# Optimization experiments

Measured on AMD Instinct MI355X. Metric: run time of the kernel, lower is better.

Reference implementation:

```python
import jax, jax.numpy as jnp
import numpy as np

B = 65536
V = 7          # vertices
OPD = 48       # op_embedding_dim
ND = 48        # node_embedding_dim
HID = 96       # hid_dim
GD = 128       # gcn out dim
NOPS = 32      # op embedding table size
NONE_OP = 3
MLP_DIMS = [200, 200, 200]


def _flow(y, adj, op_emb, W, attW, attb, bias):
    # DenseGraphFlow: support = y @ W; out = sigmoid(op_emb @ attW + attb) * (adj @ support) + support + bias
    support = jnp.einsum('bvi,io->bvo', y, W)
    gate = jax.nn.sigmoid(jnp.einsum('bve,eo->bvo', op_emb, attW) + attb)
    return gate * jnp.einsum('bvw,bwo->bvo', adj, support) + support + bias


def _forward(x_adj_1, zcp, op_emb_table, input_op_emb, output_op_emb,
             input_node_emb, other_node_emb, xh_W, xh_b,
             gcn0_W, gcn0_attW, gcn0_attb, gcn0_bias,
             gcn_W, gcn_attW, gcn_attb, gcn_bias,
             mlp0_W, mlp0_b, mlp1_W, mlp1_b, mlp2_W, mlp2_b, mlp3_W, mlp3_b,
             x_ops_1):
    b = x_ops_1.shape[0]
    adjs = jnp.transpose(x_adj_1, (0, 2, 1))              # archs use arch.T
    op_inds = x_ops_1[:, 1:-1]                            # [B, V-2]
    mid_op = op_emb_table[op_inds]                        # [B, V-2, OPD]
    op_embs = jnp.concatenate([
        jnp.broadcast_to(input_op_emb[None], (b, 1, OPD)),
        mid_op,
        jnp.broadcast_to(output_op_emb[None], (b, 1, OPD)),
    ], axis=1)                                            # [B, V, OPD]
    node_embs = jnp.concatenate([
        jnp.broadcast_to(input_node_emb[None], (b, 1, ND)),
        jnp.broadcast_to(other_node_emb[None], (b, V - 1, ND)),
    ], axis=1)                                            # [B, V, ND]
    x = jnp.einsum('bvn,nh->bvh', node_embs, xh_W) + xh_b  # [B, V, HID]

    # GCN stack: layer 0 (HID->GD), then 4 layers (GD->GD); relu except last
    y = _flow(x, adjs, op_embs, gcn0_W, gcn0_attW, gcn0_attb, gcn0_bias)
    y = jax.nn.relu(y)
    n_rest = gcn_W.shape[0]
    for i in range(n_rest):
        y = _flow(y, adjs, op_embs, gcn_W[i], gcn_attW[i], gcn_attb[i], gcn_bias[i])
        if i != n_rest - 1:
            y = jax.nn.relu(y)

    # final process: drop input node, mask none-ops, mean over nodes
    y = y[:, 1:, :]                                       # [B, V-1, GD]
    mask = (op_inds != NONE_OP).astype(jnp.float32)[:, :, None]
    y = jnp.concatenate([y[:, :-1, :] * mask, y[:, -1:, :]], axis=1)
    y = jnp.mean(y, axis=1)                               # [B, GD]

    # MLP head (dropout inactive / eval)
    y = jax.nn.relu(y @ mlp0_W + mlp0_b)
    y = jax.nn.relu(y @ mlp1_W + mlp1_b)
    y = jax.nn.relu(y @ mlp2_W + mlp2_b)
    y = y @ mlp3_W + mlp3_b                               # [B, 1]
    return y


def setup_inputs() -> dict:
    key = jax.random.key(0)
    ks = iter(jax.random.split(key, 40))
    u = lambda shape, s: jax.random.uniform(next(ks), shape, jnp.float32, -s, s)
    inp = {}
    inp['x_ops_1'] = jax.random.randint(next(ks), (B, V), 0, NOPS, dtype=jnp.int64)
    inp['x_adj_1'] = jax.random.uniform(next(ks), (B, V, V), jnp.float32)
    inp['zcp'] = jax.random.normal(next(ks), (B, 13), jnp.float32)
    inp['op_emb_table'] = jax.random.normal(next(ks), (NOPS, OPD), jnp.float32)
    inp['input_op_emb'] = jnp.zeros((1, OPD), jnp.float32)
    inp['output_op_emb'] = jax.random.normal(next(ks), (1, OPD), jnp.float32)
    inp['input_node_emb'] = jax.random.normal(next(ks), (1, ND), jnp.float32)
    inp['other_node_emb'] = jnp.zeros((1, ND), jnp.float32)
    inp['xh_W'] = u((ND, HID), 1.0 / np.sqrt(ND))
    inp['xh_b'] = u((HID,), 1.0 / np.sqrt(ND))
    s = 1.0 / np.sqrt(GD)
    inp['gcn0_W'] = u((HID, GD), s)
    inp['gcn0_attW'] = u((OPD, GD), 1.0 / np.sqrt(OPD))
    inp['gcn0_attb'] = u((GD,), 1.0 / np.sqrt(OPD))
    inp['gcn0_bias'] = u((GD,), s)
    inp['gcn_W'] = u((4, GD, GD), s)
    inp['gcn_attW'] = u((4, OPD, GD), 1.0 / np.sqrt(OPD))
    inp['gcn_attb'] = u((4, GD), 1.0 / np.sqrt(OPD))
    inp['gcn_bias'] = u((4, GD), s)
    d = GD
    for i, h in enumerate(MLP_DIMS):
        inp[f'mlp{i}_W'] = u((d, h), 1.0 / np.sqrt(d))
        inp[f'mlp{i}_b'] = u((h,), 1.0 / np.sqrt(d))
        d = h
    inp['mlp3_W'] = u((d, 1), 1.0 / np.sqrt(d))
    inp['mlp3_b'] = u((1,), 1.0 / np.sqrt(d))
    return inp


def reference(x_ops_1, x_adj_1, zcp, op_emb_table, input_op_emb, output_op_emb,
              input_node_emb, other_node_emb, xh_W, xh_b,
              gcn0_W, gcn0_attW, gcn0_attb, gcn0_bias,
              gcn_W, gcn_attW, gcn_attb, gcn_bias,
              mlp0_W, mlp0_b, mlp1_W, mlp1_b, mlp2_W, mlp2_b, mlp3_W, mlp3_b):
    return _forward(x_adj_1, zcp, op_emb_table, input_op_emb, output_op_emb,
                    input_node_emb, other_node_emb, xh_W, xh_b,
                    gcn0_W, gcn0_attW, gcn0_attb, gcn0_bias,
                    gcn_W, gcn_attW, gcn_attb, gcn_bias,
                    mlp0_W, mlp0_b, mlp1_W, mlp1_b, mlp2_W, mlp2_b, mlp3_W, mlp3_b,
                    x_ops_1)
```

## Files before the change

kernel.cpp:

```cpp
#include <hip/hip_runtime.h>
#include <math.h>

#define V 7
#define OPD 48
#define HID 96
#define GD 128
#define NGATE 34
#define NONE_OP 3
#define NB 16

typedef unsigned short u16;
typedef unsigned int u32;
typedef _Float16 f16;
typedef __attribute__((ext_vector_type(4))) _Float16 f16x4;
typedef __attribute__((ext_vector_type(8))) _Float16 f16x8;
typedef __attribute__((ext_vector_type(4))) float f32x4;

#define RSCALE 2048.0f
#define RINV   (1.0f/2048.0f)

#define WS_GATES   0u
#define WS_SUP0T   87040u
#define WS_GWH     91136u
#define WS_GWL     222208u
#define WS_W0H     353280u
#define WS_W0L     406528u
#define WS_W1H     459776u
#define WS_W1L     552960u
#define WS_W2H     646144u
#define WS_W2L     739328u

#define S_YH   0u
#define S_YL   32768u
#define S_SUPT 0u
#define S_ADJ  65536u
#define S_GI   69120u
#define S_TOTAL 69632u
#define S_ZH   0u
#define S_ZL   4096u
#define S_A1H  8192u
#define S_A1L  16384u
#define S_A2H  24576u

__device__ __forceinline__ u32 sw256(u32 row, u32 kb) { return row * 256u + (kb ^ ((row & 7u) << 4)); }
__device__ __forceinline__ u32 sw512(u32 row, u32 kb) { return row * 512u + (kb ^ ((row & 7u) << 4)); }
__device__ __forceinline__ u32 ssw(u32 col, u32 rb) { return col * 512u + (rb ^ (((col ^ (col >> 3)) & 7u) << 4)); }

#define MFMA(a, b, c) __builtin_amdgcn_mfma_f32_16x16x32_f16(a, b, c, 0, 0, 0)

__global__ __launch_bounds__(256) void precompute_kernel(
    const float* __restrict__ op_tbl, const float* __restrict__ in_op,
    const float* __restrict__ out_op, const float* __restrict__ in_node,
    const float* __restrict__ other_node, const float* __restrict__ xh_W,
    const float* __restrict__ xh_b, const float* __restrict__ g0W,
    const float* __restrict__ g0attW, const float* __restrict__ g0attb,
    const float* __restrict__ gattW, const float* __restrict__ gattb,
    const float* __restrict__ gW, const float* __restrict__ m0W,
    const float* __restrict__ m1W, const float* __restrict__ m2W,
    char* __restrict__ ws)
{
  const int blk = blockIdx.x, tid = threadIdx.x;
  float* gates = (float*)(ws + WS_GATES);
  float* sup0T = (float*)(ws + WS_SUP0T);
  if (blk < 85) {
    const int row = blk * 2 + (tid >> 7);
    const int c = tid & 127;
    const int l = row / NGATE, e = row % NGATE;
    const float* emb = (e < 32) ? (op_tbl + e * OPD) : (e == 32 ? in_op : out_op);
    const float* aW = (l == 0) ? g0attW : (gattW + (size_t)(l - 1) * OPD * GD);
    const float* ab = (l == 0) ? g0attb : (gattb + (l - 1) * GD);
    float acc = ab[c];
    for (int j = 0; j < OPD; j++) acc += emb[j] * aW[j * GD + c];
    gates[(size_t)row * GD + c] = 1.0f / (1.0f + expf(-acc));
  } else if (blk == 85) {
    __shared__ float x[V * HID];
    for (int i = tid; i < V * HID; i += 256) {
      const int v = i / HID, h = i % HID;
      const float* emb = (v == 0) ? in_node : other_node;
      float acc = xh_b[h];
      for (int j = 0; j < 48; j++) acc += emb[j] * xh_W[j * HID + h];
      x[i] = acc;
    }
    __syncthreads();
    for (int i = tid; i < V * GD; i += 256) {
      const int v = i / GD, c = i % GD;
      float acc = 0.f;
      for (int h = 0; h < HID; h++) acc += x[v * HID + h] * g0W[h * GD + c];
      sup0T[c * 8 + v] = acc;
    }
    for (int i = tid; i < GD; i += 256) sup0T[i * 8 + 7] = 0.f;
  } else {
    for (int idx = (blk - 86) * 256 + tid; idx < 185344; idx += 128 * 256) {
      float w; f16 *ph, *pl;
      if (idx < 65536) {
        const int l = idx >> 14, rem = idx & 16383;
        const int n = rem >> 7, k = rem & 127;
        w = gW[(size_t)l * 16384 + k * 128 + n];
        ph = (f16*)(ws + WS_GWH) + idx; pl = (f16*)(ws + WS_GWL) + idx;
      } else if (idx < 92160) {
        const int j = idx - 65536, n = j >> 7, k = j & 127;
        w = (n < 200) ? m0W[(size_t)k * 200 + n] : 0.f;
        ph = (f16*)(ws + WS_W0H) + j; pl = (f16*)(ws + WS_W0L) + j;
      } else if (idx < 138752) {
        const int j = idx - 92160, n = j / 224, k = j % 224;
        w = (n < 200 && k < 200) ? m1W[(size_t)k * 200 + n] : 0.f;
        ph = (f16*)(ws + WS_W1H) + j; pl = (f16*)(ws + WS_W1L) + j;
      } else {
        const int j = idx - 138752, n = j / 224, k = j % 224;
        w = (n < 200 && k < 200) ? m2W[(size_t)k * 200 + n] : 0.f;
        ph = (f16*)(ws + WS_W2H) + j; pl = (f16*)(ws + WS_W2L) + j;
      }
      const f16 h = (f16)w;
      *ph = h;
      *pl = (f16)((w - (float)h) * RSCALE);
    }
  }
}

__global__ __launch_bounds__(512, 4) void gin_main_kernel(
    const int* __restrict__ x_ops, const float* __restrict__ x_adj,
    const char* __restrict__ ws,
    const float* __restrict__ g0_bias, const float* __restrict__ gcn_bias,
    const float* __restrict__ m0b, const float* __restrict__ m1b,
    const float* __restrict__ m2b, const float* __restrict__ m3W,
    const float* __restrict__ m3b, float* __restrict__ out)
{
  extern __shared__ char smem[];
  const int tid = threadIdx.x;
  const int bbase = blockIdx.x * NB;
  const float* gates_ws = (const float*)(ws + WS_GATES);
  const float* sup0T = (const float*)(ws + WS_SUP0T);
  const f16* GWH = (const f16*)(ws + WS_GWH);
  const f16* GWL = (const f16*)(ws + WS_GWL);
  const f16* W0H = (const f16*)(ws + WS_W0H);
  const f16* W0L = (const f16*)(ws + WS_W0L);
  const f16* W1H = (const f16*)(ws + WS_W1H);
  const f16* W1L = (const f16*)(ws + WS_W1L);
  const f16* W2H = (const f16*)(ws + WS_W2H);
  const f16* W2L = (const f16*)(ws + WS_W2L);

  for (int i = tid; i < NB * 56; i += 512) {
    const int s = i / 56, r = i % 56, v = r >> 3, w = r & 7;
    ((float*)(smem + S_ADJ))[i] = (w < 7) ? x_adj[(size_t)(bbase + s) * 49 + w * 7 + v] : 0.f;
  }
  if (tid < 128) {
    const int s = tid >> 3, v = tid & 7;
    const int g = (v == 0) ? 32 : (v == 6) ? 33 : (v == 7) ? 0
                : x_ops[(size_t)(bbase + s) * 7 + v];
    ((int*)(smem + S_GI))[tid] = g;
  }
  __syncthreads();

  const int lane = tid & 63, wave = tid >> 6;
  const int lrow = lane & 15, lq = lane >> 4;
  const int ms = tid >> 5;
  const int colbase = (tid & 31) * 4;

  for (int l = 0; l < 5; l++) {
    if (l > 0) {
      const f16* wh = GWH + (l - 1) * 16384;
      const f16* wl = GWL + (l - 1) * 16384;
      f32x4 acc0[8], acc1[8];
#pragma unroll
      for (int t = 0; t < 8; t++) {
        acc0[t] = (f32x4){0.f, 0.f, 0.f, 0.f};
        acc1[t] = (f32x4){0.f, 0.f, 0.f, 0.f};
      }
#pragma unroll
      for (int ks = 0; ks < 4; ks++) {
        const int eo = (wave * 16 + lrow) * 128 + ks * 32 + lq * 8;
        const f16x8 bh = *(const f16x8*)(wh + eo);
        const f16x8 bl = *(const f16x8*)(wl + eo);
#pragma unroll
        for (int t = 0; t < 8; t++) {
          const u32 off = sw256((u32)(t * 16 + lrow), (u32)(ks * 64 + lq * 16));
          const f16x8 ah = *(const f16x8*)(smem + S_YH + off);
          const f16x8 al = *(const f16x8*)(smem + S_YL + off);
          acc0[t] = MFMA(ah, bh, acc0[t]);
          acc1[t] = MFMA(ah, bl, acc1[t]);
          acc1[t] = MFMA(al, bh, acc1[t]);
        }
      }
      __syncthreads();
      {
        const u32 col = (u32)(wave * 16 + lrow);
#pragma unroll
        for (int t = 0; t < 8; t++) {
          f32x4 vv;
#pragma unroll
          for (int r = 0; r < 4; r++) vv[r] = acc0[t][r] + acc1[t][r] * RINV;
          *(f32x4*)(smem + S_SUPT + ssw(col, (u32)(t * 64 + lq * 16))) = vv;
        }
      }
      __syncthreads();
    }

    f32x4 sa[4], sb[4];
    if (l == 0) {
#pragma unroll
      for (int c = 0; c < 4; c++) {
        const float* p = sup0T + (size_t)(colbase + c) * 8;
        sa[c] = *(const f32x4*)p;
        sb[c] = *(const f32x4*)(p + 4);
      }
    } else {
#pragma unroll
      for (int c = 0; c < 4; c++) {
        const u32 col = (u32)(colbase + c);
        sa[c] = *(const f32x4*)(smem + S_SUPT + ssw(col, (u32)(ms * 32)));
        sb[c] = *(const f32x4*)(smem + S_SUPT + ssw(col, (u32)(ms * 32 + 16)));
      }
      __syncthreads();
    }

    {
      const float* bias_l = (l == 0) ? g0_bias : gcn_bias + (l - 1) * GD;
      const f32x4 bb = *(const f32x4*)(bias_l + colbase);
      const int* giv = (const int*)(smem + S_GI) + ms * 8;
      float zacc[4];
#pragma unroll
      for (int c = 0; c < 4; c++) zacc[c] = 0.f;
#pragma unroll
      for (int v = 0; v < 7; v++) {
        const f32x4 a0 = *(const f32x4*)(smem + S_ADJ + (ms * 56 + v * 8) * 4);
        const f32x4 a1 = *(const f32x4*)(smem + S_ADJ + (ms * 56 + v * 8) * 4 + 16);
        const int gidx = giv[v];
        const f32x4 gg = *(const f32x4*)(gates_ws + ((size_t)l * NGATE + gidx) * GD + colbase);
        float y[4];
#pragma unroll
        for (int c = 0; c < 4; c++) {
          const float t = a0[0] * sa[c][0] + a0[1] * sa[c][1] + a0[2] * sa[c][2] + a0[3] * sa[c][3]
                        + a1[0] * sb[c][0] + a1[1] * sb[c][1] + a1[2] * sb[c][2];
          const float sv = (v < 4) ? sa[c][v] : sb[c][v - 4];
          y[c] = gg[c] * t + sv + bb[c];
        }
        if (l < 4) {
          union { f16x4 v4; f16 e[4]; } ph, pl;
#pragma unroll
          for (int c = 0; c < 4; c++) {
            const float r = fmaxf(y[c], 0.f);
            const f16 h = (f16)r;
            ph.e[c] = h;
            pl.e[c] = (f16)((r - (float)h) * RSCALE);
          }
          const u32 yo = sw256((u32)(ms * 8 + v), (u32)(colbase * 2));
          *(f16x4*)(smem + S_YH + yo) = ph.v4;
          *(f16x4*)(smem + S_YL + yo) = pl.v4;
        } else {
          if ((v == 6) || (v >= 1 && gidx != NONE_OP))
#pragma unroll
            for (int c = 0; c < 4; c++) zacc[c] += y[c];
        }
      }
      if (l == 4) {
        union { f16x4 v4; f16 e[4]; } ph, pl;
#pragma unroll
        for (int c = 0; c < 4; c++) {
          const float z = zacc[c] * (1.f / 6.f);
          const f16 h = (f16)z;
          ph.e[c] = h;
          pl.e[c] = (f16)((z - (float)h) * RSCALE);
        }
        const u32 zo = sw256((u32)ms, (u32)(colbase * 2));
        *(f16x4*)(smem + S_ZH + zo) = ph.v4;
        *(f16x4*)(smem + S_ZL + zo) = pl.v4;
        for (int i = tid; i < 6144; i += 512)
          ((u32*)(smem + S_A1H))[i] = 0u;
      }
    }
    __syncthreads();
  }

  {
    f32x4 macc0[2], macc1[2];
#pragma unroll
    for (int i = 0; i < 2; i++) { macc0[i] = (f32x4){0.f,0.f,0.f,0.f}; macc1[i] = (f32x4){0.f,0.f,0.f,0.f}; }
#pragma unroll
    for (int ks = 0; ks < 4; ks++) {
      const u32 off = sw256((u32)lrow, (u32)(ks * 64 + lq * 16));
      const f16x8 zh = *(const f16x8*)(smem + S_ZH + off);
      const f16x8 zl = *(const f16x8*)(smem + S_ZL + off);
#pragma unroll
      for (int i = 0; i < 2; i++) {
        const int nt = wave + i * 8;
        if (nt < 13) {
          const int eo = (nt * 16 + lrow) * 128 + ks * 32 + lq * 8;
          const f16x8 wh8 = *(const f16x8*)(W0H + eo);
          const f16x8 wl8 = *(const f16x8*)(W0L + eo);
          macc0[i] = MFMA(zh, wh8, macc0[i]);
          macc1[i] = MFMA(zh, wl8, macc1[i]);
          macc1[i] = MFMA(zl, wh8, macc1[i]);
        }
      }
    }
#pragma unroll
    for (int i = 0; i < 2; i++) {
      const int nt = wave + i * 8;
      if (nt < 13) {
        const int col = nt * 16 + lrow;
        const float b = (col < 200) ? m0b[col] : 0.f;
#pragma unroll
        for (int r = 0; r < 4; r++) {
          const float a = fmaxf(macc0[i][r] + macc1[i][r] * RINV + b, 0.f);
          const f16 h = (f16)a;
          const u32 off = sw512((u32)(lq * 4 + r), (u32)(2 * col));
          *(f16*)(smem + S_A1H + off) = h;
          *(f16*)(smem + S_A1L + off) = (f16)((a - (float)h) * RSCALE);
        }
      }
    }
  }
  __syncthreads();
  {
    f32x4 macc0[2], macc1[2];
#pragma unroll
    for (int i = 0; i < 2; i++) { macc0[i] = (f32x4){0.f,0.f,0.f,0.f}; macc1[i] = (f32x4){0.f,0.f,0.f,0.f}; }
#pragma unroll
    for (int ks = 0; ks < 7; ks++) {
      const u32 off = sw512((u32)lrow, (u32)(ks * 64 + lq * 16));
      const f16x8 ah = *(const f16x8*)(smem + S_A1H + off);
      const f16x8 al = *(const f16x8*)(smem + S_A1L + off);
#pragma unroll
      for (int i = 0; i < 2; i++) {
        const int nt = wave + i * 8;
        if (nt < 13) {
          const int eo = (nt * 16 + lrow) * 224 + ks * 32 + lq * 8;
          const f16x8 wh8 = *(const f16x8*)(W1H + eo);
          const f16x8 wl8 = *(const f16x8*)(W1L + eo);
          macc0[i] = MFMA(ah, wh8, macc0[i]);
          macc1[i] = MFMA(ah, wl8, macc1[i]);
          macc1[i] = MFMA(al, wh8, macc1[i]);
        }
      }
    }
    __syncthreads();
#pragma unroll
    for (int i = 0; i < 2; i++) {
      const int nt = wave + i * 8;
      if (nt < 13) {
        const int col = nt * 16 + lrow;
        const float b = (col < 200) ? m1b[col] : 0.f;
#pragma unroll
        for (int r = 0; r < 4; r++) {
          const float a = fmaxf(macc0[i][r] + macc1[i][r] * RINV + b, 0.f);
          const u32 off = sw512((u32)(lq * 4 + r), (u32)(2 * col));
          *(f16*)(smem + S_A2H + off) = (f16)a;
        }
      }
    }
  }
  __syncthreads();
  {
    f32x4 macc0[2], macc1[2];
#pragma unroll
    for (int i = 0; i < 2; i++) { macc0[i] = (f32x4){0.f,0.f,0.f,0.f}; macc1[i] = (f32x4){0.f,0.f,0.f,0.f}; }
#pragma unroll
    for (int ks = 0; ks < 7; ks++) {
      const u32 off = sw512((u32)lrow, (u32)(ks * 64 + lq * 16));
      const f16x8 ah = *(const f16x8*)(smem + S_A2H + off);
#pragma unroll
      for (int i = 0; i < 2; i++) {
        const int nt = wave + i * 8;
        if (nt < 13) {
          const int eo = (nt * 16 + lrow) * 224 + ks * 32 + lq * 8;
          const f16x8 wh8 = *(const f16x8*)(W2H + eo);
          const f16x8 wl8 = *(const f16x8*)(W2L + eo);
          macc0[i] = MFMA(ah, wh8, macc0[i]);
          macc1[i] = MFMA(ah, wl8, macc1[i]);
        }
      }
    }
#pragma unroll
    for (int i = 0; i < 2; i++) {
      const int nt = wave + i * 8;
      if (nt < 13) {
        const int col = nt * 16 + lrow;
        const float b = (col < 200) ? m2b[col] : 0.f;
#pragma unroll
        for (int r = 0; r < 4; r++) {
          const float a = fmaxf(macc0[i][r] + macc1[i][r] * RINV + b, 0.f);
          const u32 off = sw512((u32)(lq * 4 + r), (u32)(2 * col));
          *(f16*)(smem + S_A1H + off) = (f16)a;
        }
      }
    }
  }
  __syncthreads();
  {
    const int kl = tid & 31;
    float p = 0.f;
    for (int k = kl; k < 200; k += 32) {
      const u32 off = sw512((u32)ms, (u32)(2 * k));
      p += (float)(*(const f16*)(smem + S_A1H + off)) * m3W[k];
    }
#pragma unroll
    for (int d = 16; d > 0; d >>= 1) p += __shfl_down(p, d, 32);
    if (kl == 0) out[bbase + ms] = p + m3b[0];
  }
}

extern "C" void kernel_launch(void* const* d_in, const int* in_sizes, int n_in,
                              void* d_out, int out_size, void* d_ws, size_t ws_size,
                              hipStream_t stream) {
  const int*   x_ops    = (const int*)  d_in[0];
  const float* x_adj    = (const float*)d_in[1];
  const float* op_tbl   = (const float*)d_in[3];
  const float* in_op    = (const float*)d_in[4];
  const float* out_op   = (const float*)d_in[5];
  const float* in_node  = (const float*)d_in[6];
  const float* oth_node = (const float*)d_in[7];
  const float* xh_W     = (const float*)d_in[8];
  const float* xh_b     = (const float*)d_in[9];
  const float* g0W      = (const float*)d_in[10];
  const float* g0attW   = (const float*)d_in[11];
  const float* g0attb   = (const float*)d_in[12];
  const float* g0bias   = (const float*)d_in[13];
  const float* gW       = (const float*)d_in[14];
  const float* gattW    = (const float*)d_in[15];
  const float* gattb    = (const float*)d_in[16];
  const float* gbias    = (const float*)d_in[17];
  const float* m0W = (const float*)d_in[18], *m0b = (const float*)d_in[19];
  const float* m1W = (const float*)d_in[20], *m1b = (const float*)d_in[21];
  const float* m2W = (const float*)d_in[22], *m2b = (const float*)d_in[23];
  const float* m3W = (const float*)d_in[24], *m3b = (const float*)d_in[25];
  float* out = (float*)d_out;
  char* ws = (char*)d_ws;
  (void)ws_size; (void)n_in; (void)out_size;

  const int B = in_sizes[0] / V;
  const int nblk = B / NB;

  hipFuncSetAttribute((const void*)gin_main_kernel,
                      hipFuncAttributeMaxDynamicSharedMemorySize, (int)S_TOTAL);

  hipLaunchKernelGGL(precompute_kernel, dim3(214), dim3(256), 0, stream,
                     op_tbl, in_op, out_op, in_node, oth_node, xh_W, xh_b,
                     g0W, g0attW, g0attb, gattW, gattb, gW, m0W, m1W, m2W, ws);
  hipLaunchKernelGGL(gin_main_kernel, dim3(nblk), dim3(512), (int)S_TOTAL, stream,
                     x_ops, x_adj, (const char*)ws, g0bias, gbias,
                     m0b, m1b, m2b, m3W, m3b, out);
}
```

Measured before the change: 465.1 us.

## Apply adjacency aggregation directly on MFMA accumulators, skipping LDS support transpose

The support matrix from the MFMA is no longer written to LDS in transposed form and read back. Each lane now computes the adjacency-weighted sum over the nodes it holds straight from its accumulator registers, and gets the other half-graph's contribution with a cross-lane shuffle. This removes an LDS round trip and a barrier per layer. In exchange the epilogue writes scalar f16 values instead of f16x4 vectors and does more gate loads per element, and the adjacency buffer is padded to 8x8.

New measurement: 819.0 us. +76.1%, slower.

```diff
diff --git a/kernel.cpp b/kernel.cpp
--- a/kernel.cpp
+++ b/kernel.cpp
@@ -12,7 +12,6 @@
 typedef unsigned short u16;
 typedef unsigned int u32;
 typedef _Float16 f16;
-typedef __attribute__((ext_vector_type(4))) _Float16 f16x4;
 typedef __attribute__((ext_vector_type(8))) _Float16 f16x8;
 typedef __attribute__((ext_vector_type(4))) float f32x4;
 
@@ -32,10 +31,9 @@
 
 #define S_YH   0u
 #define S_YL   32768u
-#define S_SUPT 0u
 #define S_ADJ  65536u
-#define S_GI   69120u
-#define S_TOTAL 69632u
+#define S_GI   69632u
+#define S_TOTAL 70144u
 #define S_ZH   0u
 #define S_ZL   4096u
 #define S_A1H  8192u
@@ -44,7 +42,6 @@
 
 __device__ __forceinline__ u32 sw256(u32 row, u32 kb) { return row * 256u + (kb ^ ((row & 7u) << 4)); }
 __device__ __forceinline__ u32 sw512(u32 row, u32 kb) { return row * 512u + (kb ^ ((row & 7u) << 4)); }
-__device__ __forceinline__ u32 ssw(u32 col, u32 rb) { return col * 512u + (rb ^ (((col ^ (col >> 3)) & 7u) << 4)); }
 
 #define MFMA(a, b, c) __builtin_amdgcn_mfma_f32_16x16x32_f16(a, b, c, 0, 0, 0)
 
@@ -139,9 +136,10 @@
   const f16* W2H = (const f16*)(ws + WS_W2H);
   const f16* W2L = (const f16*)(ws + WS_W2L);
 
-  for (int i = tid; i < NB * 56; i += 512) {
-    const int s = i / 56, r = i % 56, v = r >> 3, w = r & 7;
-    ((float*)(smem + S_ADJ))[i] = (w < 7) ? x_adj[(size_t)(bbase + s) * 49 + w * 7 + v] : 0.f;
+  for (int i = tid; i < NB * 64; i += 512) {
+    const int s = i >> 6, r = i & 63, v = r >> 3, w = r & 7;
+    ((float*)(smem + S_ADJ))[i] =
+        (v < 7 && w < 7) ? x_adj[(size_t)(bbase + s) * 49 + w * 7 + v] : 0.f;
   }
   if (tid < 128) {
     const int s = tid >> 3, v = tid & 7;
@@ -153,14 +151,18 @@
 
   const int lane = tid & 63, wave = tid >> 6;
   const int lrow = lane & 15, lq = lane >> 4;
-  const int ms = tid >> 5;
-  const int colbase = (tid & 31) * 4;
+  const int h = lq & 1, hp = lq >> 1;
+  const int c = wave * 16 + lrow;
+  const u32 cb2 = (u32)(2 * c);
+  const float* adj_lds = (const float*)(smem + S_ADJ);
+  const int* giv_lds = (const int*)(smem + S_GI);
+
+  f32x4 acc0[8], acc1[8];
 
   for (int l = 0; l < 5; l++) {
     if (l > 0) {
       const f16* wh = GWH + (l - 1) * 16384;
       const f16* wl = GWL + (l - 1) * 16384;
-      f32x4 acc0[8], acc1[8];
 #pragma unroll
       for (int t = 0; t < 8; t++) {
         acc0[t] = (f32x4){0.f, 0.f, 0.f, 0.f};
@@ -168,7 +170,7 @@
       }
 #pragma unroll
       for (int ks = 0; ks < 4; ks++) {
-        const int eo = (wave * 16 + lrow) * 128 + ks * 32 + lq * 8;
+        const int eo = c * 128 + ks * 32 + lq * 8;
         const f16x8 bh = *(const f16x8*)(wh + eo);
         const f16x8 bl = *(const f16x8*)(wl + eo);
 #pragma unroll
@@ -182,91 +184,62 @@
         }
       }
       __syncthreads();
-      {
-        const u32 col = (u32)(wave * 16 + lrow);
-#pragma unroll
-        for (int t = 0; t < 8; t++) {
-          f32x4 vv;
-#pragma unroll
-          for (int r = 0; r < 4; r++) vv[r] = acc0[t][r] + acc1[t][r] * RINV;
-          *(f32x4*)(smem + S_SUPT + ssw(col, (u32)(t * 64 + lq * 16))) = vv;
-        }
-      }
-      __syncthreads();
-    }
-
-    f32x4 sa[4], sb[4];
-    if (l == 0) {
-#pragma unroll
-      for (int c = 0; c < 4; c++) {
-        const float* p = sup0T + (size_t)(colbase + c) * 8;
-        sa[c] = *(const f32x4*)p;
-        sb[c] = *(const f32x4*)(p + 4);
-      }
+#pragma unroll
+      for (int t = 0; t < 8; t++)
+#pragma unroll
+        for (int r = 0; r < 4; r++) acc0[t][r] += acc1[t][r] * RINV;
     } else {
-#pragma unroll
-      for (int c = 0; c < 4; c++) {
-        const u32 col = (u32)(colbase + c);
-        sa[c] = *(const f32x4*)(smem + S_SUPT + ssw(col, (u32)(ms * 32)));
-        sb[c] = *(const f32x4*)(smem + S_SUPT + ssw(col, (u32)(ms * 32 + 16)));
-      }
-      __syncthreads();
-    }
-
-    {
-      const float* bias_l = (l == 0) ? g0_bias : gcn_bias + (l - 1) * GD;
-      const f32x4 bb = *(const f32x4*)(bias_l + colbase);
-      const int* giv = (const int*)(smem + S_GI) + ms * 8;
-      float zacc[4];
-#pragma unroll
-      for (int c = 0; c < 4; c++) zacc[c] = 0.f;
-#pragma unroll
-      for (int v = 0; v < 7; v++) {
-        const f32x4 a0 = *(const f32x4*)(smem + S_ADJ + (ms * 56 + v * 8) * 4);
-        const f32x4 a1 = *(const f32x4*)(smem + S_ADJ + (ms * 56 + v * 8) * 4 + 16);
-        const int gidx = giv[v];
-        const f32x4 gg = *(const f32x4*)(gates_ws + ((size_t)l * NGATE + gidx) * GD + colbase);
-        float y[4];
-#pragma unroll
-        for (int c = 0; c < 4; c++) {
-          const float t = a0[0] * sa[c][0] + a0[1] * sa[c][1] + a0[2] * sa[c][2] + a0[3] * sa[c][3]
-                        + a1[0] * sb[c][0] + a1[1] * sb[c][1] + a1[2] * sb[c][2];
-          const float sv = (v < 4) ? sa[c][v] : sb[c][v - 4];
-          y[c] = gg[c] * t + sv + bb[c];
-        }
+      const f32x4 s0 = *(const f32x4*)(sup0T + (size_t)c * 8 + h * 4);
+#pragma unroll
+      for (int t = 0; t < 8; t++) acc0[t] = s0;
+    }
+
+    const float bias_c = (l == 0) ? g0_bias[c] : gcn_bias[(l - 1) * GD + c];
+    const float* gl = gates_ws + (size_t)l * NGATE * GD;
+
+#pragma unroll
+    for (int t = 0; t < 8; t++) {
+      const int s = 2 * t + hp;
+      const float* adjb = adj_lds + s * 64 + h * 4;
+      float Ps[4], Po[4];
+#pragma unroll
+      for (int rp = 0; rp < 4; rp++) {
+        const f32x4 As = *(const f32x4*)(adjb + (4 * h + rp) * 8);
+        const f32x4 Ao = *(const f32x4*)(adjb + (4 - 4 * h + rp) * 8);
+        Ps[rp] = As[0]*acc0[t][0] + As[1]*acc0[t][1] + As[2]*acc0[t][2] + As[3]*acc0[t][3];
+        Po[rp] = Ao[0]*acc0[t][0] + Ao[1]*acc0[t][1] + Ao[2]*acc0[t][2] + Ao[3]*acc0[t][3];
+      }
+      float zp = 0.f;
+#pragma unroll
+      for (int rp = 0; rp < 4; rp++) {
+        const float full = Ps[rp] + __shfl_xor(Po[rp], 16);
+        const int v = 4 * h + rp;
+        const int gidx = giv_lds[s * 8 + v];
+        const float g = gl[(size_t)gidx * GD + c];
+        const float y = g * full + acc0[t][rp] + bias_c;
         if (l < 4) {
-          union { f16x4 v4; f16 e[4]; } ph, pl;
-#pragma unroll
-          for (int c = 0; c < 4; c++) {
-            const float r = fmaxf(y[c], 0.f);
-            const f16 h = (f16)r;
-            ph.e[c] = h;
-            pl.e[c] = (f16)((r - (float)h) * RSCALE);
-          }
-          const u32 yo = sw256((u32)(ms * 8 + v), (u32)(colbase * 2));
-          *(f16x4*)(smem + S_YH + yo) = ph.v4;
-          *(f16x4*)(smem + S_YL + yo) = pl.v4;
+          const float rl = fmaxf(y, 0.f);
+          const f16 hi = (f16)rl;
+          const u32 off = sw256((u32)(t * 16 + lq * 4 + rp), cb2);
+          *(f16*)(smem + S_YH + off) = hi;
+          *(f16*)(smem + S_YL + off) = (f16)((rl - (float)hi) * RSCALE);
         } else {
-          if ((v == 6) || (v >= 1 && gidx != NONE_OP))
-#pragma unroll
-            for (int c = 0; c < 4; c++) zacc[c] += y[c];
+          const bool keep = (v == 6) || (v >= 1 && v <= 5 && gidx != NONE_OP);
+          zp += keep ? y : 0.f;
         }
       }
       if (l == 4) {
-        union { f16x4 v4; f16 e[4]; } ph, pl;
-#pragma unroll
-        for (int c = 0; c < 4; c++) {
-          const float z = zacc[c] * (1.f / 6.f);
-          const f16 h = (f16)z;
-          ph.e[c] = h;
-          pl.e[c] = (f16)((z - (float)h) * RSCALE);
-        }
-        const u32 zo = sw256((u32)ms, (u32)(colbase * 2));
-        *(f16x4*)(smem + S_ZH + zo) = ph.v4;
-        *(f16x4*)(smem + S_ZL + zo) = pl.v4;
-        for (int i = tid; i < 6144; i += 512)
-          ((u32*)(smem + S_A1H))[i] = 0u;
-      }
+        const float zf = (zp + __shfl_xor(zp, 16)) * (1.f / 6.f);
+        if (h == 0) {
+          const f16 hi = (f16)zf;
+          const u32 off = sw256((u32)s, cb2);
+          *(f16*)(smem + S_ZH + off) = hi;
+          *(f16*)(smem + S_ZL + off) = (f16)((zf - (float)hi) * RSCALE);
+        }
+      }
+    }
+    if (l == 4) {
+      for (int i = tid; i < 6144; i += 512) ((u32*)(smem + S_A1H))[i] = 0u;
     }
     __syncthreads();
   }
@@ -302,10 +275,10 @@
 #pragma unroll
         for (int r = 0; r < 4; r++) {
           const float a = fmaxf(macc0[i][r] + macc1[i][r] * RINV + b, 0.f);
-          const f16 h = (f16)a;
+          const f16 hi = (f16)a;
           const u32 off = sw512((u32)(lq * 4 + r), (u32)(2 * col));
-          *(f16*)(smem + S_A1H + off) = h;
-          *(f16*)(smem + S_A1L + off) = (f16)((a - (float)h) * RSCALE);
+          *(f16*)(smem + S_A1H + off) = hi;
+          *(f16*)(smem + S_A1L + off) = (f16)((a - (float)hi) * RSCALE);
         }
       }
     }
@@ -387,6 +360,7 @@
   }
   __syncthreads();
   {
+    const int ms = tid >> 5;
     const int kl = tid & 31;
     float p = 0.f;
     for (int k = kl; k < 200; k += 32) {
```
